# Kernel tuning notes

Hardware: AMD Instinct MI355X
Metric: run time of the kernel (lower is better)

Reference implementation:

```python
import jax, jax.numpy as jnp
import numpy as np

COMMITMENT_COST = 0.25
EMBEDDING_DIM = 64
NUM_EMBEDDINGS = 512
BATCH, SEQ = 64, 4096


def setup_inputs() -> dict:
    key = jax.random.key(0)
    k1, k2, k3 = jax.random.split(key, 3)
    return {
        "inputs": jax.random.normal(k1, (BATCH, SEQ, EMBEDDING_DIM), dtype=jnp.float32),
        "embedding": jax.random.normal(k2, (NUM_EMBEDDINGS, EMBEDDING_DIM), dtype=jnp.float32),
        "ema_cluster_size": jax.random.uniform(k3, (NUM_EMBEDDINGS,), dtype=jnp.float32),
    }


def reference(inputs, embedding, ema_cluster_size):
    # inputs: [B, T, D]; embedding: [K, D]; ema_cluster_size: [K]
    input_shape = inputs.shape
    flat = inputs.reshape(-1, EMBEDDING_DIM)  # [N, D]
    distances = (
        jnp.sum(flat * flat, axis=1, keepdims=True)
        + jnp.sum(embedding * embedding, axis=1)[None, :]
        - 2.0 * (flat @ embedding.T)
    )
    # cluster-size weighting (as in the source module)
    distances = distances * jnp.sqrt(ema_cluster_size)[None, :]
    encoding_indices = jnp.argmin(distances, axis=1)  # [N]
    # one-hot @ codebook == gather
    quantized = embedding[encoding_indices].reshape(input_shape)
    e_latent_loss = jnp.mean((jax.lax.stop_gradient(quantized) - inputs) ** 2)
    loss = COMMITMENT_COST * e_latent_loss
    # straight-through estimator
    quantized_st = inputs + jax.lax.stop_gradient(quantized - inputs)
    return quantized_st, loss, encoding_indices[:, None]
```

## Files before the change

kernel.cpp:

```cpp
#include <hip/hip_runtime.h>
#include <math.h>

#define D 64
#define K 512

typedef __attribute__((ext_vector_type(8))) short short8;
typedef __attribute__((ext_vector_type(4))) float f32x4;

#define WS_E2    256
#define WS_SQ    2304
#define WS_ETS   4352
#define WS_BP    8448
#define WS_WL    139520
#define WS_PART  1188096
#define WS_PART2 1204480

#define KEYMASK 0xFFFFFE00u
#define DIST_BIAS 0.0625f

__device__ __forceinline__ unsigned short f32_to_bf16_rne(float f)
{
    unsigned int u = __float_as_uint(f);
    unsigned int r = (u + 0x7FFFu + ((u >> 16) & 1u)) >> 16;
    return (unsigned short)r;
}
__device__ __forceinline__ float bf16_to_f32(unsigned short h)
{
    return __uint_as_float(((unsigned int)h) << 16);
}

__device__ __forceinline__ float np_sumsq64(const float* v)
{
#pragma clang fp contract(off)
    float p[64];
#pragma unroll
    for (int i = 0; i < 64; ++i) p[i] = v[i] * v[i];
    float r[8];
#pragma unroll
    for (int j = 0; j < 8; ++j) r[j] = p[j];
#pragma unroll
    for (int b = 8; b < 64; b += 8) {
#pragma unroll
        for (int j = 0; j < 8; ++j) r[j] += p[b + j];
    }
    return ((r[0] + r[1]) + (r[2] + r[3])) + ((r[4] + r[5]) + (r[6] + r[7]));
}

__global__ __launch_bounds__(256) void vq_pack_prep(
    const float* __restrict__ emb,
    const float* __restrict__ cs,
    unsigned short* __restrict__ Bp,
    float* __restrict__ e2,
    float* __restrict__ sq,
    float2* __restrict__ ets,
    int* __restrict__ cnt)
{
    int i = blockIdx.x * blockDim.x + threadIdx.x;
    if (i < 65536) {
        int j    = i & 7;
        int lane = (i >> 3) & 63;
        int frag = (i >> 9) & 3;
        int t    = (i >> 11) & 31;
        int kc   = frag & 1;
        int sB   = frag >> 1;
        int code = t * 16 + (lane & 15);
        int d    = kc * 32 + (lane >> 4) * 8 + j;
        float v = emb[code * 64 + d];
        unsigned short b0 = f32_to_bf16_rne(v);
        Bp[i] = (sB == 0) ? b0 : f32_to_bf16_rne(v - bf16_to_f32(b0));
    } else if (i < 66048) {
        int k = i - 65536;
        float er[64];
        const float* ek = emb + (size_t)k * D;
#pragma unroll
        for (int d = 0; d < 64; ++d) er[d] = ek[d];
        float e2v = np_sumsq64(er);
        float sqv = (float)sqrt((double)cs[k]);
        e2[k] = e2v;
        sq[k] = sqv;
        ets[k] = make_float2(e2v * sqv + DIST_BIAS, 2.0f * sqv);
    } else if (i == 66048) {
        *cnt = 0;
    }
}

__global__ __launch_bounds__(512) void vq_screen(
    const float* __restrict__ x,
    const float* __restrict__ emb,
    const float2* __restrict__ ets,
    const unsigned short* __restrict__ Bp,
    float* __restrict__ out_q,
    float* __restrict__ out_idx,
    int* __restrict__ wl,
    int* __restrict__ cnt,
    double* __restrict__ partial)
{
    __shared__ unsigned short BpS[65536];
    __shared__ double ls[8];

    const int wave = threadIdx.x >> 6;
    const int lane = threadIdx.x & 63;
    const int quad = lane >> 4;
    const int n16  = lane & 15;

    {
        const float4* src = (const float4*)Bp;
        float4* dst = (float4*)BpS;
#pragma unroll
        for (int it = 0; it < 16; ++it)
            dst[threadIdx.x + it * 512] = src[threadIdx.x + it * 512];
    }
    __syncthreads();

    double s = 0.0;

    for (int pass = 0; pass < 2; ++pass) {
        const int n0 = blockIdx.x * 512 + pass * 256 + wave * 32;

        short8 A0[2][2], A1[2][2];
        f32x4 negx2h[2];
#pragma unroll
        for (int rt = 0; rt < 2; ++rt) {
            float sx = 0.0f;
#pragma unroll
            for (int kc = 0; kc < 2; ++kc) {
                const float* src = x + (size_t)(n0 + rt * 16 + n16) * 64
                                   + kc * 32 + quad * 8;
                float4 v0 = *(const float4*)(src);
                float4 v1 = *(const float4*)(src + 4);
                float xv[8] = {v0.x, v0.y, v0.z, v0.w, v1.x, v1.y, v1.z, v1.w};
#pragma unroll
                for (int j = 0; j < 8; ++j) {
                    float v = xv[j];
                    unsigned short b0 = f32_to_bf16_rne(v);
                    unsigned short b1 = f32_to_bf16_rne(v - bf16_to_f32(b0));
                    A0[rt][kc][j] = (short)b0;
                    A1[rt][kc][j] = (short)b1;
                    sx = fmaf(v, v, sx);
                }
            }
            sx += __shfl_xor(sx, 16, 64);
            sx += __shfl_xor(sx, 32, 64);
#pragma unroll
            for (int r = 0; r < 4; ++r)
                negx2h[rt][r] = -0.5f * __shfl(sx, quad * 4 + r, 64);
        }

        unsigned k1[2][4], k2[2][4];
#pragma unroll
        for (int rt = 0; rt < 2; ++rt)
#pragma unroll
            for (int r = 0; r < 4; ++r) { k1[rt][r] = 0xFFFFFFFFu; k2[rt][r] = 0xFFFFFFFFu; }

#pragma unroll 2
        for (int t = 0; t < 32; ++t) {
            const unsigned short* bp = BpS + t * 2048 + lane * 8;
            const short8 B00 = *(const short8*)(bp);
            const short8 B01 = *(const short8*)(bp + 512);
            const short8 B10 = *(const short8*)(bp + 1024);
            const short8 B11 = *(const short8*)(bp + 1536);
            float2 et = ets[t * 16 + n16];
            unsigned cbits = (unsigned)(t * 16 + n16);

#pragma unroll
            for (int rt = 0; rt < 2; ++rt) {
                f32x4 acc = negx2h[rt];
                acc = __builtin_amdgcn_mfma_f32_16x16x32_bf16(A0[rt][0], B00, acc, 0, 0, 0);
                acc = __builtin_amdgcn_mfma_f32_16x16x32_bf16(A0[rt][1], B01, acc, 0, 0, 0);
                acc = __builtin_amdgcn_mfma_f32_16x16x32_bf16(A0[rt][0], B10, acc, 0, 0, 0);
                acc = __builtin_amdgcn_mfma_f32_16x16x32_bf16(A0[rt][1], B11, acc, 0, 0, 0);
                acc = __builtin_amdgcn_mfma_f32_16x16x32_bf16(A1[rt][0], B00, acc, 0, 0, 0);
                acc = __builtin_amdgcn_mfma_f32_16x16x32_bf16(A1[rt][1], B01, acc, 0, 0, 0);

#pragma unroll
                for (int r = 0; r < 4; ++r) {
                    float dist = fmaf(-et.y, acc[r], et.x);
                    unsigned key = (__float_as_uint(dist) & KEYMASK) | cbits;
                    unsigned a1 = k1[rt][r];
                    unsigned a2;
                    asm("v_med3_u32 %0, %1, %2, %3"
                        : "=v"(a2) : "v"(a1), "v"(k2[rt][r]), "v"(key));
                    k2[rt][r] = a2;
                    k1[rt][r] = a1 < key ? a1 : key;
                }
            }
        }

#pragma unroll
        for (int rt = 0; rt < 2; ++rt)
#pragma unroll
            for (int r = 0; r < 4; ++r) {
                unsigned a1 = k1[rt][r], a2 = k2[rt][r];
#pragma unroll
                for (int w = 1; w < 16; w <<= 1) {
                    unsigned o1 = (unsigned)__shfl_xor((int)a1, w, 64);
                    unsigned o2 = (unsigned)__shfl_xor((int)a2, w, 64);
                    unsigned mx  = a1 > o1 ? a1 : o1;
                    a1 = a1 < o1 ? a1 : o1;
                    unsigned mn2 = a2 < o2 ? a2 : o2;
                    a2 = mn2 < mx ? mn2 : mx;
                }
                k1[rt][r] = a1; k2[rt][r] = a2;
            }

        unsigned pk[2][4];
#pragma unroll
        for (int rt = 0; rt < 2; ++rt)
#pragma unroll
            for (int r = 0; r < 4; ++r) {
                float d1f = __uint_as_float(k1[rt][r] & KEYMASK);
                float d2f = __uint_as_float(k2[rt][r] & KEYMASK);
                int   i1  = (int)(k1[rt][r] & 0x1FFu);
                int   flg = (d2f - d1f) <= (0.01f + 2.0e-4f * d2f);
                pk[rt][r] = (unsigned)i1 | (flg ? 0x8000u : 0u);
                if (n16 == 0) {
                    int p = n0 + rt * 16 + quad * 4 + r;
                    out_idx[p] = (float)i1;
                    if (flg) { int slot = atomicAdd(cnt, 1); wl[slot] = p; }
                }
            }

        int src = (n16 >> 2) * 16 + n16;
#pragma unroll
        for (int rt = 0; rt < 2; ++rt) {
            unsigned p0 = (unsigned)__shfl((int)pk[rt][0], src, 64);
            unsigned p1 = (unsigned)__shfl((int)pk[rt][1], src, 64);
            unsigned p2 = (unsigned)__shfl((int)pk[rt][2], src, 64);
            unsigned p3 = (unsigned)__shfl((int)pk[rt][3], src, 64);
            int rr = n16 & 3;
            unsigned pm = (rr == 0) ? p0 : (rr == 1) ? p1 : (rr == 2) ? p2 : p3;
            int bim = (int)(pm & 0x1FFu);
            int flg = (int)((pm >> 15) & 1u);
            if (!flg) {
                int prow = n0 + rt * 16 + n16;
#pragma unroll
                for (int kc = 0; kc < 2; ++kc) {
                    const float* xs = x   + (size_t)prow * 64 + kc * 32 + quad * 8;
                    const float* es = emb + (size_t)bim  * 64 + kc * 32 + quad * 8;
                    float4 xv0 = *(const float4*)(xs);
                    float4 xv1 = *(const float4*)(xs + 4);
                    float4 ev0 = *(const float4*)(es);
                    float4 ev1 = *(const float4*)(es + 4);
                    float4 o0, o1;
                    float t0, t1, t2, t3, t4, t5, t6, t7;
                    {
#pragma clang fp contract(off)
                        t0 = ev0.x - xv0.x; o0.x = xv0.x + t0;
                        t1 = ev0.y - xv0.y; o0.y = xv0.y + t1;
                        t2 = ev0.z - xv0.z; o0.z = xv0.z + t2;
                        t3 = ev0.w - xv0.w; o0.w = xv0.w + t3;
                        t4 = ev1.x - xv1.x; o1.x = xv1.x + t4;
                        t5 = ev1.y - xv1.y; o1.y = xv1.y + t5;
                        t6 = ev1.z - xv1.z; o1.z = xv1.z + t6;
                        t7 = ev1.w - xv1.w; o1.w = xv1.w + t7;
                    }
                    float* od = out_q + (size_t)prow * 64 + kc * 32 + quad * 8;
                    *(float4*)(od)     = o0;
                    *(float4*)(od + 4) = o1;
                    s += (double)t0 * t0 + (double)t1 * t1
                       + (double)t2 * t2 + (double)t3 * t3
                       + (double)t4 * t4 + (double)t5 * t5
                       + (double)t6 * t6 + (double)t7 * t7;
                }
            }
        }
    }

#pragma unroll
    for (int off = 32; off > 0; off >>= 1)
        s += __shfl_down(s, off, 64);
    if (lane == 0) ls[wave] = s;
    __syncthreads();
    if (threadIdx.x == 0)
        partial[blockIdx.x] = ls[0] + ls[1] + ls[2] + ls[3]
                            + ls[4] + ls[5] + ls[6] + ls[7];
}

__global__ __launch_bounds__(256) void vq_exact(
    const float* __restrict__ x,
    const float* __restrict__ emb,
    const float* __restrict__ e2,
    const float* __restrict__ sq,
    const int* __restrict__ wl,
    const int* __restrict__ cnt,
    float* __restrict__ out_idx,
    float* __restrict__ out_q,
    double* __restrict__ partial2)
{
    const int lane = threadIdx.x & 63;
    const int gw   = blockIdx.x * 4 + (threadIdx.x >> 6);
    const int nw   = gridDim.x * 4;
    const int cv   = *cnt;

    for (int w = gw; w < cv; w += nw) {
        int p = wl[w];
        const float* xrow = x + (size_t)p * 64;
        float row[64];
#pragma unroll
        for (int i = 0; i < 16; ++i) {
            float4 v = ((const float4*)xrow)[i];
            row[4 * i + 0] = v.x; row[4 * i + 1] = v.y;
            row[4 * i + 2] = v.z; row[4 * i + 3] = v.w;
        }
        float x2 = np_sumsq64(row);

        float bd = INFINITY;
        int   bc = 0;
        for (int t = 0; t < 8; ++t) {
            int c = t * 64 + lane;
            const float* er = emb + (size_t)c * 64;
            float acc = 0.0f;
#pragma unroll
            for (int d = 0; d < 64; ++d)
                acc = fmaf(row[d], er[d], acc);
            float dist;
            {
#pragma clang fp contract(off)
                dist = ((x2 + e2[c]) - 2.0f * acc) * sq[c];
            }
            if (dist < bd) { bd = dist; bc = c; }
        }
#pragma unroll
        for (int wd = 1; wd < 64; wd <<= 1) {
            float od = __shfl_xor(bd, wd, 64);
            int   oc = __shfl_xor(bc, wd, 64);
            if (od < bd || (od == bd && oc < bc)) { bd = od; bc = oc; }
        }
        if (lane == 0) out_idx[p] = (float)bc;

        float xv = x[(size_t)p * 64 + lane];
        float qv = emb[(size_t)bc * 64 + lane];
        float t, o;
        {
#pragma clang fp contract(off)
            t = qv - xv;
            o = xv + t;
        }
        out_q[(size_t)p * 64 + lane] = o;
        double dd = (double)t * (double)t;
#pragma unroll
        for (int off = 32; off > 0; off >>= 1)
            dd += __shfl_down(dd, off, 64);
        if (lane == 0) partial2[w] = dd;
    }
}

__global__ __launch_bounds__(256) void vq_finalize(
    const double* __restrict__ partial,
    const double* __restrict__ partial2,
    const int* __restrict__ cnt,
    float* __restrict__ loss_out,
    int nblk, double inv_count)
{
    double s = 0.0;
    for (int i = threadIdx.x; i < nblk; i += 256) s += partial[i];
    int cv = *cnt;
    for (int w = threadIdx.x; w < cv; w += 256) s += partial2[w];
#pragma unroll
    for (int off = 32; off > 0; off >>= 1)
        s += __shfl_down(s, off, 64);
    __shared__ double ls[4];
    if ((threadIdx.x & 63) == 0) ls[threadIdx.x >> 6] = s;
    __syncthreads();
    if (threadIdx.x == 0) {
        double total = ls[0] + ls[1] + ls[2] + ls[3];
        loss_out[0] = (float)(0.25 * total * inv_count);
    }
}

extern "C" void kernel_launch(void* const* d_in, const int* in_sizes, int n_in,
                              void* d_out, int out_size, void* d_ws, size_t ws_size,
                              hipStream_t stream)
{
    const float* x   = (const float*)d_in[0];
    const float* emb = (const float*)d_in[1];
    const float* cs  = (const float*)d_in[2];

    const int N = in_sizes[0] / D;

    float* out      = (float*)d_out;
    float* out_q    = out;
    float* out_loss = out + (size_t)N * D;
    float* out_idx  = out_loss + 1;

    char* ws = (char*)d_ws;
    int*            cnt      = (int*)ws;
    float*          e2       = (float*)(ws + WS_E2);
    float*          sq       = (float*)(ws + WS_SQ);
    float2*         ets      = (float2*)(ws + WS_ETS);
    unsigned short* Bp       = (unsigned short*)(ws + WS_BP);
    int*            wl       = (int*)(ws + WS_WL);
    double*         partial  = (double*)(ws + WS_PART);
    double*         partial2 = (double*)(ws + WS_PART2);

    const int nblk_screen = N / 512;

    vq_pack_prep<<<259, 256, 0, stream>>>(emb, cs, Bp, e2, sq, ets, cnt);
    vq_screen<<<nblk_screen, 512, 0, stream>>>(x, emb, ets, Bp,
                                               out_q, out_idx, wl, cnt, partial);
    vq_exact<<<512, 256, 0, stream>>>(x, emb, e2, sq, wl, cnt,
                                      out_idx, out_q, partial2);
    vq_finalize<<<1, 256, 0, stream>>>(partial, partial2, cnt, out_loss,
                                       nblk_screen, 1.0 / ((double)N * (double)D));
}
```

Measured before the change: 210.0 us.

## Split quantized output emission out of screening kernel into separate grid-stride kernel

```diff
diff --git a/kernel.cpp b/kernel.cpp
--- a/kernel.cpp
+++ b/kernel.cpp
@@ -86,17 +86,13 @@
 
 __global__ __launch_bounds__(512) void vq_screen(
     const float* __restrict__ x,
-    const float* __restrict__ emb,
     const float2* __restrict__ ets,
     const unsigned short* __restrict__ Bp,
-    float* __restrict__ out_q,
     float* __restrict__ out_idx,
     int* __restrict__ wl,
-    int* __restrict__ cnt,
-    double* __restrict__ partial)
+    int* __restrict__ cnt)
 {
     __shared__ unsigned short BpS[65536];
-    __shared__ double ls[8];
 
     const int wave = threadIdx.x >> 6;
     const int lane = threadIdx.x & 63;
@@ -111,8 +107,6 @@
             dst[threadIdx.x + it * 512] = src[threadIdx.x + it * 512];
     }
     __syncthreads();
-
-    double s = 0.0;
 
     for (int pass = 0; pass < 2; ++pass) {
         const int n0 = blockIdx.x * 512 + pass * 256 + wave * 32;
@@ -203,77 +197,79 @@
                 k1[rt][r] = a1; k2[rt][r] = a2;
             }
 
-        unsigned pk[2][4];
 #pragma unroll
         for (int rt = 0; rt < 2; ++rt)
 #pragma unroll
             for (int r = 0; r < 4; ++r) {
-                float d1f = __uint_as_float(k1[rt][r] & KEYMASK);
-                float d2f = __uint_as_float(k2[rt][r] & KEYMASK);
-                int   i1  = (int)(k1[rt][r] & 0x1FFu);
-                int   flg = (d2f - d1f) <= (0.01f + 2.0e-4f * d2f);
-                pk[rt][r] = (unsigned)i1 | (flg ? 0x8000u : 0u);
                 if (n16 == 0) {
+                    float d1f = __uint_as_float(k1[rt][r] & KEYMASK);
+                    float d2f = __uint_as_float(k2[rt][r] & KEYMASK);
+                    int   i1  = (int)(k1[rt][r] & 0x1FFu);
+                    int   flg = (d2f - d1f) <= (0.01f + 2.0e-4f * d2f);
                     int p = n0 + rt * 16 + quad * 4 + r;
-                    out_idx[p] = (float)i1;
+                    out_idx[p] = flg ? -1.0f : (float)i1;
                     if (flg) { int slot = atomicAdd(cnt, 1); wl[slot] = p; }
                 }
             }
-
-        int src = (n16 >> 2) * 16 + n16;
-#pragma unroll
-        for (int rt = 0; rt < 2; ++rt) {
-            unsigned p0 = (unsigned)__shfl((int)pk[rt][0], src, 64);
-            unsigned p1 = (unsigned)__shfl((int)pk[rt][1], src, 64);
-            unsigned p2 = (unsigned)__shfl((int)pk[rt][2], src, 64);
-            unsigned p3 = (unsigned)__shfl((int)pk[rt][3], src, 64);
-            int rr = n16 & 3;
-            unsigned pm = (rr == 0) ? p0 : (rr == 1) ? p1 : (rr == 2) ? p2 : p3;
-            int bim = (int)(pm & 0x1FFu);
-            int flg = (int)((pm >> 15) & 1u);
-            if (!flg) {
-                int prow = n0 + rt * 16 + n16;
-#pragma unroll
-                for (int kc = 0; kc < 2; ++kc) {
-                    const float* xs = x   + (size_t)prow * 64 + kc * 32 + quad * 8;
-                    const float* es = emb + (size_t)bim  * 64 + kc * 32 + quad * 8;
-                    float4 xv0 = *(const float4*)(xs);
-                    float4 xv1 = *(const float4*)(xs + 4);
-                    float4 ev0 = *(const float4*)(es);
-                    float4 ev1 = *(const float4*)(es + 4);
-                    float4 o0, o1;
-                    float t0, t1, t2, t3, t4, t5, t6, t7;
-                    {
+    }
+}
+
+__global__ __launch_bounds__(256) void vq_emit(
+    const float* __restrict__ x,
+    const float* __restrict__ emb,
+    const float* __restrict__ idx,
+    float* __restrict__ out_q,
+    double* __restrict__ partial,
+    int N)
+{
+    __shared__ double ls[4];
+    const int tid    = blockIdx.x * 256 + threadIdx.x;
+    const int stride = gridDim.x * 256;
+    const long njobs = (long)N * 8;
+
+    double s = 0.0;
+    for (long j = tid; j < njobs; j += stride) {
+        long p   = j >> 3;
+        int  seg = (int)(j & 7);
+        float fi = idx[p];
+        if (fi >= 0.0f) {
+            int bi = (int)fi;
+            const float* xs = x   + p * 64 + seg * 8;
+            const float* es = emb + (size_t)bi * 64 + seg * 8;
+            float4 xv0 = *(const float4*)(xs);
+            float4 xv1 = *(const float4*)(xs + 4);
+            float4 ev0 = *(const float4*)(es);
+            float4 ev1 = *(const float4*)(es + 4);
+            float4 o0, o1;
+            float t0, t1, t2, t3, t4, t5, t6, t7;
+            {
 #pragma clang fp contract(off)
-                        t0 = ev0.x - xv0.x; o0.x = xv0.x + t0;
-                        t1 = ev0.y - xv0.y; o0.y = xv0.y + t1;
-                        t2 = ev0.z - xv0.z; o0.z = xv0.z + t2;
-                        t3 = ev0.w - xv0.w; o0.w = xv0.w + t3;
-                        t4 = ev1.x - xv1.x; o1.x = xv1.x + t4;
-                        t5 = ev1.y - xv1.y; o1.y = xv1.y + t5;
-                        t6 = ev1.z - xv1.z; o1.z = xv1.z + t6;
-                        t7 = ev1.w - xv1.w; o1.w = xv1.w + t7;
-                    }
-                    float* od = out_q + (size_t)prow * 64 + kc * 32 + quad * 8;
-                    *(float4*)(od)     = o0;
-                    *(float4*)(od + 4) = o1;
-                    s += (double)t0 * t0 + (double)t1 * t1
-                       + (double)t2 * t2 + (double)t3 * t3
-                       + (double)t4 * t4 + (double)t5 * t5
-                       + (double)t6 * t6 + (double)t7 * t7;
-                }
-            }
+                t0 = ev0.x - xv0.x; o0.x = xv0.x + t0;
+                t1 = ev0.y - xv0.y; o0.y = xv0.y + t1;
+                t2 = ev0.z - xv0.z; o0.z = xv0.z + t2;
+                t3 = ev0.w - xv0.w; o0.w = xv0.w + t3;
+                t4 = ev1.x - xv1.x; o1.x = xv1.x + t4;
+                t5 = ev1.y - xv1.y; o1.y = xv1.y + t5;
+                t6 = ev1.z - xv1.z; o1.z = xv1.z + t6;
+                t7 = ev1.w - xv1.w; o1.w = xv1.w + t7;
+            }
+            float* od = out_q + p * 64 + seg * 8;
+            *(float4*)(od)     = o0;
+            *(float4*)(od + 4) = o1;
+            s += (double)t0 * t0 + (double)t1 * t1
+               + (double)t2 * t2 + (double)t3 * t3
+               + (double)t4 * t4 + (double)t5 * t5
+               + (double)t6 * t6 + (double)t7 * t7;
         }
     }
 
 #pragma unroll
     for (int off = 32; off > 0; off >>= 1)
         s += __shfl_down(s, off, 64);
-    if (lane == 0) ls[wave] = s;
+    if ((threadIdx.x & 63) == 0) ls[threadIdx.x >> 6] = s;
     __syncthreads();
     if (threadIdx.x == 0)
-        partial[blockIdx.x] = ls[0] + ls[1] + ls[2] + ls[3]
-                            + ls[4] + ls[5] + ls[6] + ls[7];
+        partial[blockIdx.x] = ls[0] + ls[1] + ls[2] + ls[3];
 }
 
 __global__ __launch_bounds__(256) void vq_exact(
@@ -394,12 +390,13 @@
     double*         partial2 = (double*)(ws + WS_PART2);
 
     const int nblk_screen = N / 512;
+    const int nblk_emit   = 2048;
 
     vq_pack_prep<<<259, 256, 0, stream>>>(emb, cs, Bp, e2, sq, ets, cnt);
-    vq_screen<<<nblk_screen, 512, 0, stream>>>(x, emb, ets, Bp,
-                                               out_q, out_idx, wl, cnt, partial);
+    vq_screen<<<nblk_screen, 512, 0, stream>>>(x, ets, Bp, out_idx, wl, cnt);
+    vq_emit<<<nblk_emit, 256, 0, stream>>>(x, emb, out_idx, out_q, partial, N);
     vq_exact<<<512, 256, 0, stream>>>(x, emb, e2, sq, wl, cnt,
                                       out_idx, out_q, partial2);
     vq_finalize<<<1, 256, 0, stream>>>(partial, partial2, cnt, out_loss,
-                                       nblk_screen, 1.0 / ((double)N * (double)D));
-}
+                                       nblk_emit, 1.0 / ((double)N * (double)D));
+}
```

Result: slower. 217.3 us (+3.5%).
